# Kernel tuning notes

Measured on AMD Instinct MI355X. Metric: run time of the kernel, lower is better.

Reference implementation:

```python
import jax, jax.numpy as jnp
import numpy as np

N_NODES = 50000
N_EDGES = 800000
IN_FEATS = 256
HIDDEN = 128
HEADS = 2
NEG_SLOPE = 0.2


def gat_conv(x, edge_index, W, att_src, att_dst, bias, heads, out_c, concat):
    """PyG-style GATConv: linear -> per-edge attention logits -> segment
    softmax over destination neighborhoods -> scatter-add aggregate.
    Self-loops are added (PyG default add_self_loops=True)."""
    N = x.shape[0]
    h = (x @ W.T).reshape(N, heads, out_c)           # [N,H,C]
    loop = jnp.arange(N)
    src = jnp.concatenate([edge_index[0], loop])      # [E+N]
    dst = jnp.concatenate([edge_index[1], loop])
    a_src = jnp.sum(h * att_src, axis=-1)             # [N,H]
    a_dst = jnp.sum(h * att_dst, axis=-1)
    alpha = a_src[src] + a_dst[dst]                   # [E+N,H]
    alpha = jax.nn.leaky_relu(alpha, NEG_SLOPE)
    amax = jax.ops.segment_max(alpha, dst, num_segments=N)
    alpha = jnp.exp(alpha - amax[dst])
    denom = jax.ops.segment_sum(alpha, dst, num_segments=N)
    alpha = alpha / denom[dst]
    msg = h[src] * alpha[..., None]                   # [E+N,H,C]
    out = jax.ops.segment_sum(msg, dst, num_segments=N)  # [N,H,C]
    if concat:
        out = out.reshape(N, heads * out_c)
    else:
        out = out.mean(axis=1)
    return out + bias


def setup_inputs() -> dict:
    key = jax.random.key(0)
    ks = jax.random.split(key, 12)
    x = jax.random.normal(ks[0], (N_NODES, IN_FEATS), dtype=jnp.float32)
    edge_index = jax.random.randint(ks[1], (2, N_EDGES), 0, N_NODES, dtype=jnp.int64)
    s = 0.1
    W1 = jax.random.normal(ks[2], (HEADS * HIDDEN, IN_FEATS), dtype=jnp.float32) * s
    att_src1 = jax.random.normal(ks[3], (1, HEADS, HIDDEN), dtype=jnp.float32) * s
    att_dst1 = jax.random.normal(ks[4], (1, HEADS, HIDDEN), dtype=jnp.float32) * s
    b1 = jnp.zeros((HEADS * HIDDEN,), dtype=jnp.float32)
    W2 = jax.random.normal(ks[5], (HIDDEN, HEADS * HIDDEN), dtype=jnp.float32) * s
    att_src2 = jax.random.normal(ks[6], (1, 1, HIDDEN), dtype=jnp.float32) * s
    att_dst2 = jax.random.normal(ks[7], (1, 1, HIDDEN), dtype=jnp.float32) * s
    b2 = jnp.zeros((HIDDEN,), dtype=jnp.float32)
    return {"x": x, "edge_index": edge_index,
            "W1": W1, "att_src1": att_src1, "att_dst1": att_dst1, "b1": b1,
            "W2": W2, "att_src2": att_src2, "att_dst2": att_dst2, "b2": b2}


def reference(x, edge_index, W1, att_src1, att_dst1, b1, W2, att_src2, att_dst2, b2):
    h = gat_conv(x, edge_index, W1, att_src1, att_dst1, b1, HEADS, HIDDEN, True)
    h = jax.nn.relu(h)
    out = gat_conv(h, edge_index, W2, att_src2, att_dst2, b2, 1, HIDDEN, False)
    return out
```

## Files before the change

### kernel.cpp

```cpp
#include <hip/hip_runtime.h>
#include <hip/hip_bf16.h>


typedef _Float16 half8v __attribute__((ext_vector_type(8)));
typedef _Float16 half4v __attribute__((ext_vector_type(4)));
typedef _Float16 half2v __attribute__((ext_vector_type(2)));
typedef float f32x4 __attribute__((ext_vector_type(4)));


template <typename TA, int H, bool SCATTER>
__global__ __launch_bounds__(256) void gemm_att_kernel(
    const TA* __restrict__ A,
    const float* __restrict__ B,
    _Float16* __restrict__ C,
    const float* __restrict__ att_s,
    const float* __restrict__ att_d,
    float* __restrict__ a_s,
    float* __restrict__ a_d,
    int M, int K, int GB,
    const int* __restrict__ esrc, const int* __restrict__ edst,
    const int* __restrict__ rank, const int* __restrict__ csr_off,
    int* __restrict__ csr_src, int E, int nScatBlk)
{
    constexpr int BM = 128, BK = 32, LDA = 40;
    constexpr int NCOL = H * 128;
    __shared__ _Float16 Ah[BM * LDA];
    __shared__ _Float16 Bh[BM * LDA];
    __shared__ float red[2][2][64][2];

    const int tid = threadIdx.x;
    const int bid = blockIdx.x;

    if constexpr (SCATTER) {
        if (bid >= GB * H) {
            const int sbid = bid - GB * H;
            const int nq = (E + 3) >> 2;
            for (int q = sbid * 256 + tid; q < nq; q += nScatBlk * 256) {
                const int e4 = q * 4;
                if (e4 + 3 < E) {
                    const int4 sv = *reinterpret_cast<const int4*>(esrc + e4);
                    const int4 dv = *reinterpret_cast<const int4*>(edst + e4);
                    const int4 rv = *reinterpret_cast<const int4*>(rank + e4);
                    csr_src[csr_off[dv.x] + 1 + rv.x] = sv.x;
                    csr_src[csr_off[dv.y] + 1 + rv.y] = sv.y;
                    csr_src[csr_off[dv.z] + 1 + rv.z] = sv.z;
                    csr_src[csr_off[dv.w] + 1 + rv.w] = sv.w;
                } else {
                    for (int k = e4; k < E; ++k)
                        csr_src[csr_off[edst[k]] + 1 + rank[k]] = esrc[k];
                }
            }
            return;
        }
    }

    const int m0 = (bid % GB) * BM;
    const int by = bid / GB;
    const int n0 = by * 128;
    const int w  = tid >> 6;
    const int l  = tid & 63;
    const int wm = (w >> 1) * 64;
    const int wn = (w & 1) * 64;
    const int lr = l & 15;
    const int lq = l >> 4;

    f32x4 acc[4][4] = {};

    for (int k0 = 0; k0 < K; k0 += BK) {
        if constexpr (__is_same(TA, float)) {
#pragma unroll
            for (int it = 0; it < 4; ++it) {
                const int row = (tid >> 3) + it * 32;
                const int gm  = min(m0 + row, M - 1);
                const int c4  = (tid & 7) * 4;
                float4 v = *reinterpret_cast<const float4*>(A + (long)gm * K + k0 + c4);
                half4v o = { (_Float16)v.x, (_Float16)v.y, (_Float16)v.z, (_Float16)v.w };
                *reinterpret_cast<half4v*>(&Ah[row * LDA + c4]) = o;
            }
        } else {
#pragma unroll
            for (int it = 0; it < 2; ++it) {
                const int row = (tid >> 2) + it * 64;
                const int gm  = min(m0 + row, M - 1);
                const int c8  = (tid & 3) * 8;
                float4 v = *reinterpret_cast<const float4*>((const char*)A + ((long)gm * K + k0 + c8) * 2);
                *reinterpret_cast<float4*>(&Ah[row * LDA + c8]) = v;
            }
        }
#pragma unroll
        for (int it = 0; it < 4; ++it) {
            const int row = (tid >> 3) + it * 32;
            const int c4  = (tid & 7) * 4;
            float4 v = *reinterpret_cast<const float4*>(B + (long)(n0 + row) * K + k0 + c4);
            half4v o = { (_Float16)v.x, (_Float16)v.y, (_Float16)v.z, (_Float16)v.w };
            *reinterpret_cast<half4v*>(&Bh[row * LDA + c4]) = o;
        }
        __syncthreads();

        half8v af[4], bf[4];
#pragma unroll
        for (int i = 0; i < 4; ++i)
            af[i] = *reinterpret_cast<const half8v*>(&Ah[(wm + i * 16 + lr) * LDA + lq * 8]);
#pragma unroll
        for (int j = 0; j < 4; ++j)
            bf[j] = *reinterpret_cast<const half8v*>(&Bh[(wn + j * 16 + lr) * LDA + lq * 8]);
#pragma unroll
        for (int i = 0; i < 4; ++i)
#pragma unroll
            for (int j = 0; j < 4; ++j)
                acc[i][j] = __builtin_amdgcn_mfma_f32_16x16x32_f16(af[i], bf[j], acc[i][j], 0, 0, 0);
        __syncthreads();
    }

#pragma unroll
    for (int i = 0; i < 4; ++i) {
        const int gm_base = m0 + wm + i * 16 + lq * 4;
#pragma unroll
        for (int r = 0; r < 4; ++r) {
            const int gm = gm_base + r;
            if (gm < M) {
#pragma unroll
                for (int j = 0; j < 4; ++j)
                    C[(long)gm * NCOL + n0 + wn + j * 16 + lr] = (_Float16)acc[i][j][r];
            }
        }
    }

    float asv[4], adv[4];
#pragma unroll
    for (int j = 0; j < 4; ++j) {
        asv[j] = att_s[n0 + wn + j * 16 + lr];
        adv[j] = att_d[n0 + wn + j * 16 + lr];
    }
    float ps[4][4] = {}, pd[4][4] = {};
#pragma unroll
    for (int i = 0; i < 4; ++i)
#pragma unroll
        for (int j = 0; j < 4; ++j)
#pragma unroll
            for (int r = 0; r < 4; ++r) {
                ps[i][r] += acc[i][j][r] * asv[j];
                pd[i][r] += acc[i][j][r] * adv[j];
            }
#pragma unroll
    for (int o = 1; o < 16; o <<= 1)
#pragma unroll
        for (int i = 0; i < 4; ++i)
#pragma unroll
            for (int r = 0; r < 4; ++r) {
                ps[i][r] += __shfl_xor(ps[i][r], o, 64);
                pd[i][r] += __shfl_xor(pd[i][r], o, 64);
            }
    if (lr == 0) {
#pragma unroll
        for (int i = 0; i < 4; ++i)
#pragma unroll
            for (int r = 0; r < 4; ++r) {
                const int row = i * 16 + lq * 4 + r;
                red[wm >> 6][wn >> 6][row][0] = ps[i][r];
                red[wm >> 6][wn >> 6][row][1] = pd[i][r];
            }
    }
    __syncthreads();
    if (wn == 0) {
        const int row = l;
        const int gm = m0 + wm + row;
        if (gm < M) {
            const int wi = wm >> 6;
            a_s[(long)gm * H + by] = red[wi][0][row][0] + red[wi][1][row][0];
            a_d[(long)gm * H + by] = red[wi][0][row][1] + red[wi][1][row][1];
        }
    }
}


__global__ void count_kernel(const int* __restrict__ dst, int* __restrict__ deg,
                             int* __restrict__ rank, int E)
{
    const int tid = blockIdx.x * blockDim.x + threadIdx.x;
    const int e4 = tid * 4;
    if (e4 + 3 < E) {
        const int4 d = *reinterpret_cast<const int4*>(dst + e4);
        int4 r;
        r.x = atomicAdd(&deg[d.x], 1);
        r.y = atomicAdd(&deg[d.y], 1);
        r.z = atomicAdd(&deg[d.z], 1);
        r.w = atomicAdd(&deg[d.w], 1);
        *reinterpret_cast<int4*>(rank + e4) = r;
    } else if (e4 < E) {
        for (int k = e4; k < E; ++k) rank[k] = atomicAdd(&deg[dst[k]], 1);
    }
}

__global__ __launch_bounds__(256) void block_scan_kernel(
    const int* __restrict__ deg, int* __restrict__ pre, int* __restrict__ blk, int n)
{
    __shared__ int s[256];
    const int t = threadIdx.x;
    const int base = blockIdx.x * 1024 + t * 4;
    int4 d = make_int4(-1, -1, -1, -1);
    if (base + 3 < n) d = *reinterpret_cast<const int4*>(deg + base);
    else {
        if (base + 0 < n) d.x = deg[base + 0];
        if (base + 1 < n) d.y = deg[base + 1];
        if (base + 2 < n) d.z = deg[base + 2];
        if (base + 3 < n) d.w = deg[base + 3];
    }
    const int v0 = d.x + 1, v1 = d.y + 1, v2 = d.z + 1, v3 = d.w + 1;
    s[t] = v0 + v1 + v2 + v3;
    __syncthreads();
#pragma unroll
    for (int o = 1; o < 256; o <<= 1) {
        int val = 0;
        if (t >= o) val = s[t - o];
        __syncthreads();
        s[t] += val;
        __syncthreads();
    }
    int run = (t == 0) ? 0 : s[t - 1];
    int4 o4;
    o4.x = run; run += v0;
    o4.y = run; run += v1;
    o4.z = run; run += v2;
    o4.w = run; run += v3;
    if (base + 3 < n) *reinterpret_cast<int4*>(pre + base) = o4;
    else {
        if (base + 0 < n) pre[base + 0] = o4.x;
        if (base + 1 < n) pre[base + 1] = o4.y;
        if (base + 2 < n) pre[base + 2] = o4.z;
        if (base + 3 < n) pre[base + 3] = o4.w;
    }
    if (t == 255) blk[blockIdx.x] = s[255];
}

__global__ __launch_bounds__(256) void finalize_scan_kernel(
    const int* __restrict__ pre, const int* __restrict__ blk,
    int* __restrict__ off, int* __restrict__ csr_src, int n, int nvb)
{
    __shared__ int s_add;
    const int vb = blockIdx.x;
    const int t  = threadIdx.x;
    if (t < 64) {
        int v = (t < vb) ? blk[t] : 0;
#pragma unroll
        for (int o = 32; o > 0; o >>= 1) v += __shfl_xor(v, o, 64);
        if (t == 0) s_add = v;
    }
    __syncthreads();
    const int add = s_add;
    const int base = vb * 1024 + t * 4;
    if (base + 3 < n) {
        int4 p = *reinterpret_cast<const int4*>(pre + base);
        p.x += add; p.y += add; p.z += add; p.w += add;
        *reinterpret_cast<int4*>(off + base) = p;
        csr_src[p.x] = base + 0;
        csr_src[p.y] = base + 1;
        csr_src[p.z] = base + 2;
        csr_src[p.w] = base + 3;
    } else {
#pragma unroll
        for (int k = 0; k < 4; ++k)
            if (base + k < n) {
                const int v = pre[base + k] + add;
                off[base + k] = v;
                csr_src[v] = base + k;
            }
    }
    if (vb == nvb - 1 && t == 0) off[n] = add + blk[vb];
}


#define AGG_TILE 64

template <int H, int C, int VPT, bool RELU, typename TOUT>
__global__ __launch_bounds__(H * C / VPT) void aggregate_kernel(
    const int* __restrict__ csr_off,
    const int* __restrict__ csr_src,
    const _Float16* __restrict__ h,
    const float* __restrict__ a_s,
    const float* __restrict__ a_d,
    const float* __restrict__ bias,
    TOUT* __restrict__ out)
{
    const int d   = blockIdx.x;
    const int t   = threadIdx.x;
    const int col = t * VPT;
    const int hh  = col / C;

    __shared__ int   s_src[AGG_TILE];
    __shared__ float s_w[AGG_TILE][H];

    const int beg = csr_off[d];
    const int end = csr_off[d + 1];

    float acc[VPT] = {};
    float wsum = 0.f;

    for (int base = beg; base < end; base += AGG_TILE) {
        const int len = min(AGG_TILE, end - base);
        if (t < len) {
            const int s = csr_src[base + t];
            s_src[t] = s;
#pragma unroll
            for (int h2 = 0; h2 < H; ++h2) {
                float logit = a_s[s * H + h2] + a_d[d * H + h2];
                logit = logit > 0.f ? logit : 0.2f * logit;
                s_w[t][h2] = __expf(logit);
            }
        }
        __syncthreads();
#pragma unroll 4
        for (int j = 0; j < len; ++j) {
            const float w = s_w[j][hh];
            const int   s = s_src[j];
            if constexpr (VPT == 4) {
                half4v hv = *reinterpret_cast<const half4v*>(h + (long)s * (H * C) + col);
                acc[0] += w * (float)hv.x;
                acc[1] += w * (float)hv.y;
                acc[2] += w * (float)hv.z;
                acc[3] += w * (float)hv.w;
            } else {
                half2v hv = *reinterpret_cast<const half2v*>(h + (long)s * (H * C) + col);
                acc[0] += w * (float)hv.x;
                acc[1] += w * (float)hv.y;
            }
            wsum += w;
        }
        __syncthreads();
    }

    const float inv = 1.f / wsum;
    float r[VPT];
#pragma unroll
    for (int k = 0; k < VPT; ++k) {
        r[k] = acc[k] * inv + bias[col + k];
        if (RELU) r[k] = r[k] > 0.f ? r[k] : 0.f;
    }
    if constexpr (__is_same(TOUT, _Float16)) {
#pragma unroll
        for (int k = 0; k < VPT; ++k)
            out[(long)d * (H * C) + col + k] = (_Float16)r[k];
    } else {
#pragma unroll
        for (int k = 0; k < VPT; ++k)
            out[(long)d * (H * C) + col + k] = r[k];
    }
}


extern "C" void kernel_launch(void* const* d_in, const int* in_sizes, int n_in,
                              void* d_out, int out_size, void* d_ws, size_t ws_size,
                              hipStream_t stream)
{
    const float* x    = (const float*)d_in[0];
    const int*   eidx = (const int*)d_in[1];
    const float* W1   = (const float*)d_in[2];
    const float* as1  = (const float*)d_in[3];
    const float* ad1  = (const float*)d_in[4];
    const float* b1   = (const float*)d_in[5];
    const float* W2   = (const float*)d_in[6];
    const float* as2  = (const float*)d_in[7];
    const float* ad2  = (const float*)d_in[8];
    const float* b2   = (const float*)d_in[9];
    float* out = (float*)d_out;

    const int IN_FEATS = 256;
    const int N = in_sizes[0] / IN_FEATS;
    const int E = in_sizes[1] / 2;

    const int* esrc = eidx;
    const int* edst = eidx + E;

    size_t off = 0;
    auto alloc = [&](size_t bytes) -> void* {
        void* p = (char*)d_ws + off;
        off += (bytes + 255) & ~(size_t)255;
        return p;
    };
    _Float16* h1h   = (_Float16*)alloc((size_t)N * 256 * 2);
    _Float16* o1h   = (_Float16*)alloc((size_t)N * 256 * 2);
    _Float16* h2h   = (_Float16*)alloc((size_t)N * 128 * 2);
    float* a1s      = (float*)alloc((size_t)N * 2 * 4);
    float* a1d      = (float*)alloc((size_t)N * 2 * 4);
    float* a2s      = (float*)alloc((size_t)N * 4);
    float* a2d      = (float*)alloc((size_t)N * 4);
    int*   deg      = (int*)alloc((size_t)N * 4);
    int*   pre      = (int*)alloc((size_t)N * 4);
    int*   rank     = (int*)alloc((size_t)E * 4);
    int*   csr_off  = (int*)alloc((size_t)(N + 1) * 4);
    int*   csr_src  = (int*)alloc((size_t)(E + N) * 4);
    int*   blk      = (int*)alloc(64 * 4);

    const int nvb = (N + 1023) / 1024;

    hipMemsetAsync(deg, 0, (size_t)N * 4, stream);
    count_kernel<<<((E + 3) / 4 + 255) / 256, 256, 0, stream>>>(edst, deg, rank, E);
    block_scan_kernel<<<nvb, 256, 0, stream>>>(deg, pre, blk, N);
    finalize_scan_kernel<<<nvb, 256, 0, stream>>>(pre, blk, csr_off, csr_src, N, nvb);

    {
        const int GB = (N + 127) / 128;
        const int nScat = 192;
        gemm_att_kernel<float, 2, true><<<GB * 2 + nScat, 256, 0, stream>>>(
            x, W1, h1h, as1, ad1, a1s, a1d, N, 256, GB,
            esrc, edst, rank, csr_off, csr_src, E, nScat);
    }
    aggregate_kernel<2, 128, 4, true, _Float16><<<N, 64, 0, stream>>>(
        csr_off, csr_src, h1h, a1s, a1d, b1, o1h);

    {
        const int GB = (N + 127) / 128;
        gemm_att_kernel<_Float16, 1, false><<<GB, 256, 0, stream>>>(
            o1h, W2, h2h, as2, ad2, a2s, a2d, N, 256, GB,
            nullptr, nullptr, nullptr, nullptr, nullptr, 0, 0);
    }
    aggregate_kernel<1, 128, 2, false, float><<<N, 64, 0, stream>>>(
        csr_off, csr_src, h2h, a2s, a2d, b2, out);
}
```

Before: 291.2 us.

## Fuse CSR build (memset, count, scan, finalize) into one cooperative kernel

Replaces the memset plus three separate CSR-construction kernels with a single cooperative kernel that uses grid-wide syncs between the zeroing, degree counting, block scan and finalize phases. This removes several launch gaps on the stream. It adds grid.sync costs and a fixed 1024-block cooperative grid that must fit co-resident. It also raises the unroll factor of the aggregation inner loop from 4 to 8.

Result: slower. 550.3 us (+89.0%).

```diff
diff --git a/kernel.cpp b/kernel.cpp
--- a/kernel.cpp
+++ b/kernel.cpp
@@ -1,11 +1,124 @@
 #include <hip/hip_runtime.h>
 #include <hip/hip_bf16.h>
+#include <hip/hip_cooperative_groups.h>
+
+namespace cg = cooperative_groups;
 
 
 typedef _Float16 half8v __attribute__((ext_vector_type(8)));
 typedef _Float16 half4v __attribute__((ext_vector_type(4)));
 typedef _Float16 half2v __attribute__((ext_vector_type(2)));
 typedef float f32x4 __attribute__((ext_vector_type(4)));
+
+
+__global__ __launch_bounds__(256) void csr_coop_kernel(
+    const int* __restrict__ dst,
+    int* __restrict__ deg, int* __restrict__ pre, int* __restrict__ blk,
+    int* __restrict__ rank, int* __restrict__ csr_off, int* __restrict__ csr_src,
+    int E, int N, int nvb)
+{
+    cg::grid_group grid = cg::this_grid();
+    const int tid  = blockIdx.x * blockDim.x + threadIdx.x;
+    const int nthr = gridDim.x * blockDim.x;
+    const int t    = threadIdx.x;
+
+    const int nz = (N + 3) / 4;
+    for (int i = tid; i < nz; i += nthr) {
+        const int b = i * 4;
+        if (b + 3 < N) *reinterpret_cast<int4*>(deg + b) = make_int4(0, 0, 0, 0);
+        else for (int k = b; k < N; ++k) deg[k] = 0;
+    }
+    grid.sync();
+
+    const int nq = (E + 3) / 4;
+    for (int q = tid; q < nq; q += nthr) {
+        const int e4 = q * 4;
+        if (e4 + 3 < E) {
+            const int4 d = *reinterpret_cast<const int4*>(dst + e4);
+            int4 r;
+            r.x = atomicAdd(&deg[d.x], 1);
+            r.y = atomicAdd(&deg[d.y], 1);
+            r.z = atomicAdd(&deg[d.z], 1);
+            r.w = atomicAdd(&deg[d.w], 1);
+            *reinterpret_cast<int4*>(rank + e4) = r;
+        } else {
+            for (int k = e4; k < E; ++k) rank[k] = atomicAdd(&deg[dst[k]], 1);
+        }
+    }
+    grid.sync();
+
+    __shared__ int s[256];
+    if (blockIdx.x < (unsigned)nvb) {
+        const int vb = blockIdx.x;
+        const int base = vb * 1024 + t * 4;
+        int4 d = make_int4(-1, -1, -1, -1);
+        if (base + 3 < N) d = *reinterpret_cast<const int4*>(deg + base);
+        else {
+            if (base + 0 < N) d.x = deg[base + 0];
+            if (base + 1 < N) d.y = deg[base + 1];
+            if (base + 2 < N) d.z = deg[base + 2];
+            if (base + 3 < N) d.w = deg[base + 3];
+        }
+        const int v0 = d.x + 1, v1 = d.y + 1, v2 = d.z + 1, v3 = d.w + 1;
+        s[t] = v0 + v1 + v2 + v3;
+        __syncthreads();
+#pragma unroll
+        for (int o = 1; o < 256; o <<= 1) {
+            int val = 0;
+            if (t >= o) val = s[t - o];
+            __syncthreads();
+            s[t] += val;
+            __syncthreads();
+        }
+        int run = (t == 0) ? 0 : s[t - 1];
+        int4 o4;
+        o4.x = run; run += v0;
+        o4.y = run; run += v1;
+        o4.z = run; run += v2;
+        o4.w = run; run += v3;
+        if (base + 3 < N) *reinterpret_cast<int4*>(pre + base) = o4;
+        else {
+            if (base + 0 < N) pre[base + 0] = o4.x;
+            if (base + 1 < N) pre[base + 1] = o4.y;
+            if (base + 2 < N) pre[base + 2] = o4.z;
+            if (base + 3 < N) pre[base + 3] = o4.w;
+        }
+        if (t == 255) blk[vb] = s[255];
+    }
+    grid.sync();
+
+    if (blockIdx.x < (unsigned)nvb) {
+        const int vb = blockIdx.x;
+        __shared__ int s_add;
+        if (t < 64) {
+            int v = (t < vb) ? blk[t] : 0;
+#pragma unroll
+            for (int o = 32; o > 0; o >>= 1) v += __shfl_xor(v, o, 64);
+            if (t == 0) s_add = v;
+        }
+        __syncthreads();
+        const int add = s_add;
+        const int base = vb * 1024 + t * 4;
+        if (base + 3 < N) {
+            int4 p = *reinterpret_cast<const int4*>(pre + base);
+            p.x += add; p.y += add; p.z += add; p.w += add;
+            *reinterpret_cast<int4*>(csr_off + base) = p;
+            csr_src[p.x] = base + 0;
+            csr_src[p.y] = base + 1;
+            csr_src[p.z] = base + 2;
+            csr_src[p.w] = base + 3;
+        } else {
+#pragma unroll
+            for (int k = 0; k < 4; ++k)
+                if (base + k < N) {
+                    const int v = pre[base + k] + add;
+                    csr_off[base + k] = v;
+                    csr_src[v] = base + k;
+                }
+        }
+        if (vb == nvb - 1 && t == 0) csr_off[N] = add + blk[vb];
+    }
+}
 
 
 template <typename TA, int H, bool SCATTER>
@@ -174,102 +287,6 @@
 }
 
 
-__global__ void count_kernel(const int* __restrict__ dst, int* __restrict__ deg,
-                             int* __restrict__ rank, int E)
-{
-    const int tid = blockIdx.x * blockDim.x + threadIdx.x;
-    const int e4 = tid * 4;
-    if (e4 + 3 < E) {
-        const int4 d = *reinterpret_cast<const int4*>(dst + e4);
-        int4 r;
-        r.x = atomicAdd(&deg[d.x], 1);
-        r.y = atomicAdd(&deg[d.y], 1);
-        r.z = atomicAdd(&deg[d.z], 1);
-        r.w = atomicAdd(&deg[d.w], 1);
-        *reinterpret_cast<int4*>(rank + e4) = r;
-    } else if (e4 < E) {
-        for (int k = e4; k < E; ++k) rank[k] = atomicAdd(&deg[dst[k]], 1);
-    }
-}
-
-__global__ __launch_bounds__(256) void block_scan_kernel(
-    const int* __restrict__ deg, int* __restrict__ pre, int* __restrict__ blk, int n)
-{
-    __shared__ int s[256];
-    const int t = threadIdx.x;
-    const int base = blockIdx.x * 1024 + t * 4;
-    int4 d = make_int4(-1, -1, -1, -1);
-    if (base + 3 < n) d = *reinterpret_cast<const int4*>(deg + base);
-    else {
-        if (base + 0 < n) d.x = deg[base + 0];
-        if (base + 1 < n) d.y = deg[base + 1];
-        if (base + 2 < n) d.z = deg[base + 2];
-        if (base + 3 < n) d.w = deg[base + 3];
-    }
-    const int v0 = d.x + 1, v1 = d.y + 1, v2 = d.z + 1, v3 = d.w + 1;
-    s[t] = v0 + v1 + v2 + v3;
-    __syncthreads();
-#pragma unroll
-    for (int o = 1; o < 256; o <<= 1) {
-        int val = 0;
-        if (t >= o) val = s[t - o];
-        __syncthreads();
-        s[t] += val;
-        __syncthreads();
-    }
-    int run = (t == 0) ? 0 : s[t - 1];
-    int4 o4;
-    o4.x = run; run += v0;
-    o4.y = run; run += v1;
-    o4.z = run; run += v2;
-    o4.w = run; run += v3;
-    if (base + 3 < n) *reinterpret_cast<int4*>(pre + base) = o4;
-    else {
-        if (base + 0 < n) pre[base + 0] = o4.x;
-        if (base + 1 < n) pre[base + 1] = o4.y;
-        if (base + 2 < n) pre[base + 2] = o4.z;
-        if (base + 3 < n) pre[base + 3] = o4.w;
-    }
-    if (t == 255) blk[blockIdx.x] = s[255];
-}
-
-__global__ __launch_bounds__(256) void finalize_scan_kernel(
-    const int* __restrict__ pre, const int* __restrict__ blk,
-    int* __restrict__ off, int* __restrict__ csr_src, int n, int nvb)
-{
-    __shared__ int s_add;
-    const int vb = blockIdx.x;
-    const int t  = threadIdx.x;
-    if (t < 64) {
-        int v = (t < vb) ? blk[t] : 0;
-#pragma unroll
-        for (int o = 32; o > 0; o >>= 1) v += __shfl_xor(v, o, 64);
-        if (t == 0) s_add = v;
-    }
-    __syncthreads();
-    const int add = s_add;
-    const int base = vb * 1024 + t * 4;
-    if (base + 3 < n) {
-        int4 p = *reinterpret_cast<const int4*>(pre + base);
-        p.x += add; p.y += add; p.z += add; p.w += add;
-        *reinterpret_cast<int4*>(off + base) = p;
-        csr_src[p.x] = base + 0;
-        csr_src[p.y] = base + 1;
-        csr_src[p.z] = base + 2;
-        csr_src[p.w] = base + 3;
-    } else {
-#pragma unroll
-        for (int k = 0; k < 4; ++k)
-            if (base + k < n) {
-                const int v = pre[base + k] + add;
-                off[base + k] = v;
-                csr_src[v] = base + k;
-            }
-    }
-    if (vb == nvb - 1 && t == 0) off[n] = add + blk[vb];
-}
-
-
 #define AGG_TILE 64
 
 template <int H, int C, int VPT, bool RELU, typename TOUT>
@@ -309,7 +326,7 @@
             }
         }
         __syncthreads();
-#pragma unroll 4
+#pragma unroll 8
         for (int j = 0; j < len; ++j) {
             const float w = s_w[j][hh];
             const int   s = s_src[j];
@@ -365,8 +382,8 @@
     float* out = (float*)d_out;
 
     const int IN_FEATS = 256;
-    const int N = in_sizes[0] / IN_FEATS;
-    const int E = in_sizes[1] / 2;
+    int N = in_sizes[0] / IN_FEATS;
+    int E = in_sizes[1] / 2;
 
     const int* esrc = eidx;
     const int* edst = eidx + E;
@@ -391,12 +408,15 @@
     int*   csr_src  = (int*)alloc((size_t)(E + N) * 4);
     int*   blk      = (int*)alloc(64 * 4);
 
-    const int nvb = (N + 1023) / 1024;
-
-    hipMemsetAsync(deg, 0, (size_t)N * 4, stream);
-    count_kernel<<<((E + 3) / 4 + 255) / 256, 256, 0, stream>>>(edst, deg, rank, E);
-    block_scan_kernel<<<nvb, 256, 0, stream>>>(deg, pre, blk, N);
-    finalize_scan_kernel<<<nvb, 256, 0, stream>>>(pre, blk, csr_off, csr_src, N, nvb);
+    int nvb = (N + 1023) / 1024;
+
+    {
+        void* args[] = { (void*)&edst, (void*)&deg, (void*)&pre, (void*)&blk,
+                         (void*)&rank, (void*)&csr_off, (void*)&csr_src,
+                         (void*)&E, (void*)&N, (void*)&nvb };
+        hipLaunchCooperativeKernel((void*)csr_coop_kernel, dim3(1024), dim3(256),
+                                   args, 0, stream);
+    }
 
     {
         const int GB = (N + 127) / 128;
```
